# Optimization experiments

Hardware: AMD Instinct MI355X
Metric: run time of the kernel (lower is better)

The kernel has to match this reference:

```python
import jax, jax.numpy as jnp
import numpy as np

# LIF constants derived from init kwargs (delta_t=1e-3, tau_mem=20e-3, tau_syn=7.5e-3, tau_ref=2.86e-3)
THR = 1.0
ALPHA = float(np.exp(-1e-3 / 20e-3))   # membrane-trace decay for P
BETA = float(np.exp(-1e-3 / 7.5e-3))   # synaptic-trace decay for Q
GAMMA = float(np.exp(-1e-3 / 2.86e-3)) # refractory decay for R
POOL = 2
PAD = 2


def _conv2d(x, w, b):
    # x: [B,Cin,H,W], w: [Cout,Cin,k,k] -> [B,Cout,H,W] (same padding=2 for k=5)
    y = jax.lax.conv_general_dilated(
        x, w, window_strides=(1, 1), padding=[(PAD, PAD), (PAD, PAD)],
        dimension_numbers=('NCHW', 'OIHW', 'NCHW'))
    return y + b[None, :, None, None]


def _maxpool(x, k):
    return jax.lax.reduce_window(x, -jnp.inf, jax.lax.max,
                                 (1, 1, k, k), (1, 1, k, k), 'VALID')


def _spike(u):
    # hard threshold with SmoothStep (boxcar) straight-through surrogate gradient
    s_hard = (u > THR).astype(u.dtype)
    surr = jnp.clip(u - THR + 0.5, 0.0, 1.0)
    return jax.lax.stop_gradient(s_hard - surr) + surr


def setup_inputs() -> dict:
    key = jax.random.key(0)
    ks = jax.random.split(key, 7)
    B, Cin, H, W = 64, 64, 64, 64
    Cout, K = 128, 5
    fan_in = K * K * Cin
    flat = Cout * (H // POOL) * (W // POOL)  # 131072
    input_t = (jax.random.uniform(ks[0], (B, Cin, H, W)) < 0.1).astype(jnp.float32)
    P = jax.random.normal(ks[1], (B, Cin, H, W), jnp.float32)
    Q = jax.random.normal(ks[2], (B, Cin, H, W), jnp.float32)
    R = jax.random.normal(ks[3], (B, Cout, H, W), jnp.float32) * 0.1
    weights = jax.random.normal(ks[4], (Cout, Cin, K, K), jnp.float32) / np.sqrt(fan_in)
    bias = jax.random.normal(ks[5], (Cout,), jnp.float32) * 0.01
    L = 0.5 / np.sqrt(flat)  # lc_ampl / sqrt(input_features)
    w_sign = jax.random.uniform(ks[6], (10, flat), jnp.float32, -L, L)
    return {"input_t": input_t, "P": P, "Q": Q, "R": R,
            "weights": weights, "bias": bias, "w_sign": w_sign}


def reference(input_t, P, Q, R, weights, bias, w_sign):
    # one LIF timestep (quantization globals are None -> quant ops are identity, scale=1)
    P_new = ALPHA * P + (1.0 - ALPHA) * Q          # membrane trace
    Q_new = BETA * Q + (1.0 - BETA) * input_t      # synaptic trace
    R_new = GAMMA * R                              # refractory decay
    U = _conv2d(P_new, weights, bias) - R_new      # membrane potential
    S = _spike(U)                                  # spikes
    flat = _maxpool(S, POOL).reshape(S.shape[0], -1)
    # QLinearFunctional with sign random weights: (x @ W^T + 1)/2
    readout = (jnp.einsum('bf,of->bo', flat, w_sign) + 1.0) * 0.5
    return (S, U, readout)
```

## Files before the change

### kernel.cpp

```cpp
#include <hip/hip_runtime.h>
#include <math.h>

#define B_    64
#define CIN   64
#define COUT  128
#define HWHW  4096
#define NPIX  (B_ * COUT * HWHW)
#define TAU   2e-4f
#define NW3   204800
#define POOLED_FLOATS (B_ * COUT * 1024)
#define PART_FLOATS   (B_ * 10 * COUT)
#define PNS   66

typedef _Float16 half8  __attribute__((ext_vector_type(8)));
typedef _Float16 half2v __attribute__((ext_vector_type(2)));
typedef float    f32x4  __attribute__((ext_vector_type(4)));
typedef float    f32x16 __attribute__((ext_vector_type(16)));

__device__ __forceinline__ void gload_lds16(const void* g, void* l)
{
    __builtin_amdgcn_global_load_lds(
        (const __attribute__((address_space(1))) unsigned int*)g,
        (__attribute__((address_space(3))) unsigned int*)l, 16, 0, 0);
}

__global__ __launch_bounds__(256) void wprep_kernel(
    const float* __restrict__ W, _Float16* __restrict__ whi,
    _Float16* __restrict__ wlo)
{
    int e = blockIdx.x * 256 + threadIdx.x;
    if (e >= NW3) return;
    int k   = e & 15;
    int co  = (e >> 4) & 127;
    int r   = e >> 11;
    int tap = r % 25;
    int cc  = r / 25;
    float w = W[(size_t)((co << 6) + (cc << 4) + k) * 25 + tap];
    _Float16 h = (_Float16)w;
    whi[e] = h;
    wlo[e] = (_Float16)(w - (float)h);
}

__global__ __launch_bounds__(256) void pnprep_kernel(
    const float* __restrict__ P, const float* __restrict__ Q,
    _Float16* __restrict__ pnh, _Float16* __restrict__ pnl,
    float alpha, float oma)
{
    const int tid = threadIdx.x;
    const int y   = blockIdx.x;
    const int b   = blockIdx.y;
    __shared__ _Float16 th[64 * PNS];
    __shared__ _Float16 tl[64 * PNS];

    const size_t rb = (size_t)b * CIN * HWHW + ((size_t)y << 6);
#pragma unroll
    for (int k = 0; k < 4; ++k) {
        int idx = tid + (k << 8);
        int cin = idx >> 4;
        int x0  = (idx & 15) << 2;
        float4 p4 = *(const float4*)(P + rb + (size_t)cin * HWHW + x0);
        float4 q4 = *(const float4*)(Q + rb + (size_t)cin * HWHW + x0);
        float pn[4] = { alpha * p4.x + oma * q4.x, alpha * p4.y + oma * q4.y,
                        alpha * p4.z + oma * q4.z, alpha * p4.w + oma * q4.w };
        half2v h0, h1, l0, l1;
        {
            _Float16 a0 = (_Float16)pn[0], a1 = (_Float16)pn[1];
            _Float16 a2 = (_Float16)pn[2], a3 = (_Float16)pn[3];
            h0[0] = a0; h0[1] = a1; h1[0] = a2; h1[1] = a3;
            l0[0] = (_Float16)(pn[0] - (float)a0);
            l0[1] = (_Float16)(pn[1] - (float)a1);
            l1[0] = (_Float16)(pn[2] - (float)a2);
            l1[1] = (_Float16)(pn[3] - (float)a3);
        }
        int base = cin * PNS + x0;
        *(half2v*)&th[base]     = h0;
        *(half2v*)&th[base + 2] = h1;
        *(half2v*)&tl[base]     = l0;
        *(half2v*)&tl[base + 2] = l1;
    }
    __syncthreads();

    const size_t ob = ((((size_t)b << 12) + ((size_t)y << 6)) << 6);
#pragma unroll
    for (int k = 0; k < 2; ++k) {
        int gg  = tid + (k << 8);
        int x   = gg >> 3;
        int oct = gg & 7;
        half8 hv, lv;
#pragma unroll
        for (int j = 0; j < 8; ++j) {
            hv[j] = th[(oct * 8 + j) * PNS + x];
            lv[j] = tl[(oct * 8 + j) * PNS + x];
        }
        *(half8*)(pnh + ob + ((size_t)x << 6) + (oct << 3)) = hv;
        *(half8*)(pnl + ob + ((size_t)x << 6) + (oct << 3)) = lv;
    }
}

struct WFrag2 { half8 h[2]; half8 l[2]; };

__global__ __launch_bounds__(256) void lif_conv_mfma_pn_kernel(
    const _Float16* __restrict__ pnh, const _Float16* __restrict__ pnl,
    const float* __restrict__ R, const _Float16* __restrict__ whi,
    const _Float16* __restrict__ wlo, const float* __restrict__ bias,
    float* __restrict__ out, float* __restrict__ pooled,
    const void* __restrict__ zp,
    unsigned* __restrict__ cnt, int* __restrict__ list, int cap,
    float gamma)
{
    const int tid  = threadIdx.x;
    const int wave = tid >> 6;
    const int lane = tid & 63;
    const int b      = blockIdx.z;
    const int cobase = blockIdx.y << 6;
    const int ty0    = (blockIdx.x >> 2) << 4;
    const int tx0    = (blockIdx.x & 3) << 4;
    const int l31    = lane & 31;
    const int loct   = lane >> 5;

    __shared__ __align__(16) _Float16 sH[416 * 16];
    __shared__ __align__(16) _Float16 sL[416 * 16];

    f32x16 acc[2][2];
#pragma unroll
    for (int i = 0; i < 2; ++i)
#pragma unroll
        for (int j = 0; j < 2; ++j)
#pragma unroll
            for (int r = 0; r < 16; ++r) acc[i][j][r] = 0.f;

    const int wlb = ((cobase + l31) << 4) + (loct << 3);

    for (int cc = 0; cc < 4; ++cc) {
        __syncthreads();
        for (int i = wave; i < 26; i += 4) {
            const int ii = (i < 13) ? i : (i - 13);
            _Float16* sbuf = (i < 13) ? sH : sL;
            const _Float16* gb = (i < 13) ? pnh : pnl;
            const int g  = (ii << 6) + lane;
            const int px = g >> 1;
            const int c  = g & 1;
            const int r  = px / 20;
            const int col = px - 20 * r;
            const int gy = ty0 - 2 + r;
            const int gx = tx0 - 2 + col;
            const void* src = zp;
            if (px < 400 && (unsigned)gy < 64u && (unsigned)gx < 64u) {
                const int cs = c ^ ((px >> 2) & 1);
                src = gb + ((((size_t)b << 12) + (gy << 6) + gx) << 6)
                         + (cc << 4) + (cs << 3);
            }
            gload_lds16(src, (char*)sbuf + (ii << 10));
        }
        __syncthreads();

        const _Float16* wh  = whi + (size_t)cc * 25 * 2048 + wlb;
        const _Float16* wl_ = wlo + (size_t)cc * 25 * 2048 + wlb;
        WFrag2 wbuf[2];
#pragma unroll
        for (int nt = 0; nt < 2; ++nt) {
            wbuf[0].h[nt] = *(const half8*)(wh + (nt << 9));
            wbuf[0].l[nt] = *(const half8*)(wl_ + (nt << 9));
        }
#pragma unroll
        for (int t = 0; t < 25; ++t) {
            {
                const int tn = (t < 24) ? (t + 1) : 24;
                WFrag2& wn = wbuf[(t + 1) & 1];
#pragma unroll
                for (int nt = 0; nt < 2; ++nt) {
                    wn.h[nt] = *(const half8*)(wh + (size_t)tn * 2048 + (nt << 9));
                    wn.l[nt] = *(const half8*)(wl_ + (size_t)tn * 2048 + (nt << 9));
                }
            }
            __builtin_amdgcn_sched_barrier(0);

            const WFrag2& w = wbuf[t & 1];
            const int dy = t / 5;
            const int dx = t - 5 * dy;

            half8 aH[2], aL[2];
#pragma unroll
            for (int mt = 0; mt < 2; ++mt) {
                const int px = ((wave << 1) + mt) << 5 | l31;
                const int hp = ((px >> 4) + dy) * 20 + (px & 15) + dx;
                int a = (hp << 5) + (loct << 4);
                a ^= ((hp >> 2) & 1) << 4;
                aH[mt] = *(const half8*)((const char*)sH + a);
                aL[mt] = *(const half8*)((const char*)sL + a);
            }

            __builtin_amdgcn_s_setprio(1);
#pragma unroll
            for (int mt = 0; mt < 2; ++mt) {
#pragma unroll
                for (int nt = 0; nt < 2; ++nt) {
                    acc[mt][nt] = __builtin_amdgcn_mfma_f32_32x32x16_f16(
                        aH[mt], w.h[nt], acc[mt][nt], 0, 0, 0);
                    acc[mt][nt] = __builtin_amdgcn_mfma_f32_32x32x16_f16(
                        aH[mt], w.l[nt], acc[mt][nt], 0, 0, 0);
                    acc[mt][nt] = __builtin_amdgcn_mfma_f32_32x32x16_f16(
                        aL[mt], w.h[nt], acc[mt][nt], 0, 0, 0);
                }
            }
            __builtin_amdgcn_s_setprio(0);
        }
    }

#pragma unroll
    for (int nt = 0; nt < 2; ++nt) {
        const int co = cobase + (nt << 5) + l31;
        const float bv = bias[co];
        const int plane = b * COUT + co;
#pragma unroll
        for (int mt = 0; mt < 2; ++mt) {
            const int m = (wave << 1) + mt;
            float us[4][4];
#pragma unroll
            for (int rg = 0; rg < 4; ++rg) {
                const int y  = ty0 + (m << 1) + (rg >> 1);
                const int xb = ((rg & 1) << 3) + (loct << 2);
                const size_t ro = ((size_t)plane << 12) + (y << 6) + tx0 + xb;
                float4 r4 = *(const float4*)&R[ro];
                us[rg][0] = acc[mt][nt][(rg << 2) + 0] + bv - gamma * r4.x;
                us[rg][1] = acc[mt][nt][(rg << 2) + 1] + bv - gamma * r4.y;
                us[rg][2] = acc[mt][nt][(rg << 2) + 2] + bv - gamma * r4.z;
                us[rg][3] = acc[mt][nt][(rg << 2) + 3] + bv - gamma * r4.w;
                float4 uq = make_float4(us[rg][0], us[rg][1], us[rg][2], us[rg][3]);
                float4 sq = make_float4(us[rg][0] > 1.f ? 1.f : 0.f,
                                        us[rg][1] > 1.f ? 1.f : 0.f,
                                        us[rg][2] > 1.f ? 1.f : 0.f,
                                        us[rg][3] > 1.f ? 1.f : 0.f);
                *(float4*)&out[ro] = sq;
                *(float4*)&out[(size_t)NPIX + ro] = uq;
#pragma unroll
                for (int j = 0; j < 4; ++j) {
                    if (fabsf(us[rg][j] - 1.f) < TAU) {
                        unsigned pos = atomicAdd(cnt, 1u);
                        if (pos < (unsigned)cap)
                            list[pos] = (int)(ro + j);
                    }
                }
            }
            const int py  = (ty0 >> 1) + m;
            const int pxb = (tx0 >> 1) + (loct << 1);
            float* pp = pooled + ((size_t)plane << 10) + (py << 5);
            float2 pA, pB;
            pA.x = (fmaxf(fmaxf(us[0][0], us[0][1]), fmaxf(us[2][0], us[2][1])) > 1.f) ? 1.f : 0.f;
            pA.y = (fmaxf(fmaxf(us[0][2], us[0][3]), fmaxf(us[2][2], us[2][3])) > 1.f) ? 1.f : 0.f;
            pB.x = (fmaxf(fmaxf(us[1][0], us[1][1]), fmaxf(us[3][0], us[3][1])) > 1.f) ? 1.f : 0.f;
            pB.y = (fmaxf(fmaxf(us[1][2], us[1][3]), fmaxf(us[3][2], us[3][3])) > 1.f) ? 1.f : 0.f;
            *(float2*)(pp + pxb) = pA;
            *(float2*)(pp + pxb + 4) = pB;
        }
    }
}

__global__ __launch_bounds__(256) void lif_conv_mfma_reg_kernel(
    const float* __restrict__ P, const float* __restrict__ Q,
    const float* __restrict__ R, const _Float16* __restrict__ whi,
    const _Float16* __restrict__ wlo, const float* __restrict__ bias,
    float* __restrict__ out, float* __restrict__ pooled,
    unsigned* __restrict__ cnt, int* __restrict__ list, int cap, int do_pool,
    float alpha, float oma, float gamma)
{
    const int tid  = threadIdx.x;
    const int wave = tid >> 6;
    const int lane = tid & 63;
    const int b      = blockIdx.z;
    const int cobase = blockIdx.y << 6;
    const int ty0    = (blockIdx.x >> 2) << 4;
    const int tx0    = (blockIdx.x & 3) << 4;
    const int l31    = lane & 31;
    const int loct   = lane >> 5;

    __shared__ __align__(16) _Float16 sH[6400];
    __shared__ __align__(16) _Float16 sL[6400];

    f32x16 acc[2][2];
#pragma unroll
    for (int i = 0; i < 2; ++i)
#pragma unroll
        for (int j = 0; j < 2; ++j)
#pragma unroll
            for (int r = 0; r < 16; ++r) acc[i][j][r] = 0.f;

    const int wlb = ((cobase + l31) << 4) + (loct << 3);

    for (int cc = 0; cc < 4; ++cc) {
        __syncthreads();
        for (int e = tid; e < 1024; e += 256) {
            int px = e & 511;
            int hh = e >> 9;
            if (px >= 400) continue;
            int r  = px / 20;
            int c_ = px - 20 * r;
            int gy = ty0 - 2 + r;
            int gx = tx0 - 2 + c_;
            half8 hv, lv;
            if ((unsigned)gy < 64u && (unsigned)gx < 64u) {
                const size_t pb = ((size_t)(b * CIN + (cc << 4) + (hh << 3)) << 12)
                                + (gy << 6) + gx;
                const float* Pp = P + pb;
                const float* Qp = Q + pb;
#pragma unroll
                for (int j = 0; j < 8; ++j) {
                    float pn = alpha * Pp[j << 12] + oma * Qp[j << 12];
                    _Float16 h = (_Float16)pn;
                    hv[j] = h;
                    lv[j] = (_Float16)(pn - (float)h);
                }
            } else {
#pragma unroll
                for (int j = 0; j < 8; ++j) { hv[j] = (_Float16)0.f; lv[j] = (_Float16)0.f; }
            }
            int a = (px << 5) + (hh << 4);
            a ^= ((px >> 2) & 1) << 4;
            *(half8*)((char*)sH + a) = hv;
            *(half8*)((char*)sL + a) = lv;
        }
        __syncthreads();

        const _Float16* wh  = whi + (size_t)cc * 25 * 2048 + wlb;
        const _Float16* wl_ = wlo + (size_t)cc * 25 * 2048 + wlb;
        WFrag2 wbuf[2];
#pragma unroll
        for (int nt = 0; nt < 2; ++nt) {
            wbuf[0].h[nt] = *(const half8*)(wh + (nt << 9));
            wbuf[0].l[nt] = *(const half8*)(wl_ + (nt << 9));
        }
#pragma unroll
        for (int t = 0; t < 25; ++t) {
            {
                const int tn = (t < 24) ? (t + 1) : 24;
                WFrag2& wn = wbuf[(t + 1) & 1];
#pragma unroll
                for (int nt = 0; nt < 2; ++nt) {
                    wn.h[nt] = *(const half8*)(wh + (size_t)tn * 2048 + (nt << 9));
                    wn.l[nt] = *(const half8*)(wl_ + (size_t)tn * 2048 + (nt << 9));
                }
            }
            __builtin_amdgcn_sched_barrier(0);

            const WFrag2& w = wbuf[t & 1];
            const int dy = t / 5;
            const int dx = t - 5 * dy;
            half8 aH[2], aL[2];
#pragma unroll
            for (int mt = 0; mt < 2; ++mt) {
                const int px = ((wave << 1) + mt) << 5 | l31;
                const int hp = ((px >> 4) + dy) * 20 + (px & 15) + dx;
                int a = (hp << 5) + (loct << 4);
                a ^= ((hp >> 2) & 1) << 4;
                aH[mt] = *(const half8*)((const char*)sH + a);
                aL[mt] = *(const half8*)((const char*)sL + a);
            }
            __builtin_amdgcn_s_setprio(1);
#pragma unroll
            for (int mt = 0; mt < 2; ++mt) {
#pragma unroll
                for (int nt = 0; nt < 2; ++nt) {
                    acc[mt][nt] = __builtin_amdgcn_mfma_f32_32x32x16_f16(
                        aH[mt], w.h[nt], acc[mt][nt], 0, 0, 0);
                    acc[mt][nt] = __builtin_amdgcn_mfma_f32_32x32x16_f16(
                        aH[mt], w.l[nt], acc[mt][nt], 0, 0, 0);
                    acc[mt][nt] = __builtin_amdgcn_mfma_f32_32x32x16_f16(
                        aL[mt], w.h[nt], acc[mt][nt], 0, 0, 0);
                }
            }
            __builtin_amdgcn_s_setprio(0);
        }
    }

#pragma unroll
    for (int nt = 0; nt < 2; ++nt) {
        const int co = cobase + (nt << 5) + l31;
        const float bv = bias[co];
        const int plane = b * COUT + co;
#pragma unroll
        for (int mt = 0; mt < 2; ++mt) {
            const int m = (wave << 1) + mt;
            float us[4][4];
#pragma unroll
            for (int rg = 0; rg < 4; ++rg) {
                const int y  = ty0 + (m << 1) + (rg >> 1);
                const int xb = ((rg & 1) << 3) + (loct << 2);
                const size_t ro = ((size_t)plane << 12) + (y << 6) + tx0 + xb;
                float4 r4 = *(const float4*)&R[ro];
                us[rg][0] = acc[mt][nt][(rg << 2) + 0] + bv - gamma * r4.x;
                us[rg][1] = acc[mt][nt][(rg << 2) + 1] + bv - gamma * r4.y;
                us[rg][2] = acc[mt][nt][(rg << 2) + 2] + bv - gamma * r4.z;
                us[rg][3] = acc[mt][nt][(rg << 2) + 3] + bv - gamma * r4.w;
                float4 uq = make_float4(us[rg][0], us[rg][1], us[rg][2], us[rg][3]);
                float4 sq = make_float4(us[rg][0] > 1.f ? 1.f : 0.f,
                                        us[rg][1] > 1.f ? 1.f : 0.f,
                                        us[rg][2] > 1.f ? 1.f : 0.f,
                                        us[rg][3] > 1.f ? 1.f : 0.f);
                *(float4*)&out[ro] = sq;
                *(float4*)&out[(size_t)NPIX + ro] = uq;
#pragma unroll
                for (int j = 0; j < 4; ++j) {
                    if (fabsf(us[rg][j] - 1.f) < TAU) {
                        unsigned pos = atomicAdd(cnt, 1u);
                        if (pos < (unsigned)cap)
                            list[pos] = (int)(ro + j);
                    }
                }
            }
            if (do_pool) {
                const int py  = (ty0 >> 1) + m;
                const int pxb = (tx0 >> 1) + (loct << 1);
                float* pp = pooled + ((size_t)plane << 10) + (py << 5);
                float2 pA, pB;
                pA.x = (fmaxf(fmaxf(us[0][0], us[0][1]), fmaxf(us[2][0], us[2][1])) > 1.f) ? 1.f : 0.f;
                pA.y = (fmaxf(fmaxf(us[0][2], us[0][3]), fmaxf(us[2][2], us[2][3])) > 1.f) ? 1.f : 0.f;
                pB.x = (fmaxf(fmaxf(us[1][0], us[1][1]), fmaxf(us[3][0], us[3][1])) > 1.f) ? 1.f : 0.f;
                pB.y = (fmaxf(fmaxf(us[1][2], us[1][3]), fmaxf(us[3][2], us[3][3])) > 1.f) ? 1.f : 0.f;
                *(float2*)(pp + pxb) = pA;
                *(float2*)(pp + pxb + 4) = pB;
            }
        }
    }
}

__global__ __launch_bounds__(256) void repair_list_kernel(
    const float* __restrict__ P, const float* __restrict__ Q,
    const float* __restrict__ R, const float* __restrict__ W,
    const float* __restrict__ bias, float* __restrict__ out,
    const unsigned* __restrict__ cnt, const int* __restrict__ list, int cap,
    double alpha, double oma, double gamma)
{
    const int nrep = (int)min(*cnt, (unsigned)cap);
    const int wid  = (blockIdx.x * 256 + threadIdx.x) >> 6;
    const int lane = threadIdx.x & 63;
    const int nw   = (gridDim.x * 256) >> 6;

    for (int i = wid; i < nrep; i += nw) {
        const int idx   = list[i];
        const int plane = idx >> 12;
        const int pix   = idx & 4095;
        const int oy    = pix >> 6;
        const int ox    = pix & 63;
        const int b     = plane >> 7;
        const int co    = plane & 127;

        const float* Pp = P + ((size_t)b * CIN + lane) * HWHW;
        const float* Qp = Q + ((size_t)b * CIN + lane) * HWHW;
        const float* Wp = W + ((size_t)co * CIN + lane) * 25;

        double acc = 0.0;
#pragma unroll
        for (int dy = 0; dy < 5; ++dy) {
            int iy = oy + dy - 2;
            if ((unsigned)iy >= 64u) continue;
#pragma unroll
            for (int dx = 0; dx < 5; ++dx) {
                int ix = ox + dx - 2;
                if ((unsigned)ix >= 64u) continue;
                int off = (iy << 6) + ix;
                double pn = alpha * (double)Pp[off] + oma * (double)Qp[off];
                acc = fma((double)Wp[dy * 5 + dx], pn, acc);
            }
        }
#pragma unroll
        for (int s = 32; s; s >>= 1) acc += __shfl_down(acc, s, 64);

        if (lane == 0) {
            double u64 = acc + (double)bias[co]
                       - gamma * (double)R[(size_t)plane * HWHW + pix];
            out[idx]                = (u64 > 1.0) ? 1.f : 0.f;
            out[(size_t)NPIX + idx] = (float)u64;
        }
    }
}

__global__ __launch_bounds__(256) void pool_fix_kernel(
    const float* __restrict__ out, float* __restrict__ pooled,
    const unsigned* __restrict__ cnt, const int* __restrict__ list, int cap)
{
    const int nrep = (int)min(*cnt, (unsigned)cap);
    for (int i = blockIdx.x * 256 + threadIdx.x; i < nrep; i += gridDim.x * 256) {
        int idx   = list[i];
        int plane = idx >> 12;
        int pix   = idx & 4095;
        int oy    = pix >> 6;
        int ox    = pix & 63;
        size_t base = ((size_t)plane << 12) + ((oy & ~1) << 6) + (ox & ~1);
        float m = fmaxf(fmaxf(out[base], out[base + 1]),
                        fmaxf(out[base + 64], out[base + 65]));
        pooled[((size_t)plane << 10) + ((oy >> 1) << 5) + (ox >> 1)] = m;
    }
}

__global__ void ro_init(float* ro)
{
    int i = blockIdx.x * 256 + threadIdx.x;
    if (i < 640) ro[i] = 0.5f;
}

__global__ __launch_bounds__(256) void readout_pooled_kernel(
    const float* __restrict__ pooled, const float* __restrict__ wsig,
    float* __restrict__ part)
{
    const int tid = threadIdx.x;
    const int c   = blockIdx.x;
    const int bg  = blockIdx.y;

    __shared__ float wl[10 * 1024];
    for (int i = tid; i < 10240; i += 256)
        wl[i] = wsig[(size_t)(i >> 10) * 131072 + (c << 10) + (i & 1023)];
    __syncthreads();

    __shared__ float psum[4][10];
    const int wave = tid >> 6;
    const int lane = tid & 63;

    for (int bi = 0; bi < 8; ++bi) {
        const int b = (bg << 3) + bi;
        const float* pp = pooled + (((size_t)b * COUT + c) << 10);
        float acc[10];
#pragma unroll
        for (int o = 0; o < 10; ++o) acc[o] = 0.f;
#pragma unroll
        for (int it = 0; it < 4; ++it) {
            int f = tid + (it << 8);
            float m = pp[f];
#pragma unroll
            for (int o = 0; o < 10; ++o)
                acc[o] = fmaf(m, wl[(o << 10) + f], acc[o]);
        }
#pragma unroll
        for (int o = 0; o < 10; ++o) {
            float v = acc[o];
            v += __shfl_down(v, 32, 64);
            v += __shfl_down(v, 16, 64);
            v += __shfl_down(v, 8, 64);
            v += __shfl_down(v, 4, 64);
            v += __shfl_down(v, 2, 64);
            v += __shfl_down(v, 1, 64);
            if (lane == 0) psum[wave][o] = v;
        }
        __syncthreads();
        if (tid < 10) {
            float s = psum[0][tid] + psum[1][tid] + psum[2][tid] + psum[3][tid];
            part[((size_t)b * 10 + tid) * 128 + c] = s;
        }
        __syncthreads();
    }
}

__global__ __launch_bounds__(256) void readout_reduce_kernel(
    const float* __restrict__ part, float* __restrict__ ro)
{
    int i = blockIdx.x * 256 + threadIdx.x;
    if (i >= 640) return;
    const float* pp = part + (size_t)i * 128;
    float s = 0.f;
#pragma unroll
    for (int c = 0; c < 128; ++c) s += pp[c];
    ro[i] = 0.5f * s + 0.5f;
}

__global__ __launch_bounds__(256) void readout_kernel(
    const float* __restrict__ S, const float* __restrict__ wsig,
    float* __restrict__ ro)
{
    const int tid = threadIdx.x;
    const int b = blockIdx.x >> 7;
    const int c = blockIdx.x & 127;

    __shared__ float wl[10 * 1024];
    for (int idx = tid; idx < 10240; idx += 256) {
        int o = idx >> 10;
        int f = idx & 1023;
        wl[idx] = wsig[(size_t)o * 131072 + (c << 10) + f];
    }
    __syncthreads();

    float acc[10];
#pragma unroll
    for (int o = 0; o < 10; ++o) acc[o] = 0.f;

    const float* Sp = S + ((size_t)b * COUT + c) * HWHW;
#pragma unroll
    for (int i = 0; i < 4; ++i) {
        int fl = tid + (i << 8);
        int ph = fl >> 5, pw = fl & 31;
        const float2 t0 = *(const float2*)&Sp[(ph << 7) + (pw << 1)];
        const float2 t1 = *(const float2*)&Sp[(ph << 7) + 64 + (pw << 1)];
        float m = fmaxf(fmaxf(t0.x, t0.y), fmaxf(t1.x, t1.y));
#pragma unroll
        for (int o = 0; o < 10; ++o)
            acc[o] = fmaf(m, wl[(o << 10) + fl], acc[o]);
    }

    __shared__ float psum[4][10];
    const int wave = tid >> 6;
    const int lane = tid & 63;
#pragma unroll
    for (int o = 0; o < 10; ++o) {
        float v = acc[o];
        v += __shfl_down(v, 32, 64);
        v += __shfl_down(v, 16, 64);
        v += __shfl_down(v, 8, 64);
        v += __shfl_down(v, 4, 64);
        v += __shfl_down(v, 2, 64);
        v += __shfl_down(v, 1, 64);
        if (lane == 0) psum[wave][o] = v;
    }
    __syncthreads();
    if (tid < 10) {
        float s = psum[0][tid] + psum[1][tid] + psum[2][tid] + psum[3][tid];
        atomicAdd(&ro[b * 10 + tid], 0.5f * s);
    }
}

extern "C" void kernel_launch(void* const* d_in, const int* in_sizes, int n_in,
                              void* d_out, int out_size, void* d_ws, size_t ws_size,
                              hipStream_t stream)
{
    const float* P    = (const float*)d_in[1];
    const float* Q    = (const float*)d_in[2];
    const float* R    = (const float*)d_in[3];
    const float* W    = (const float*)d_in[4];
    const float* bias = (const float*)d_in[5];
    const float* wsig = (const float*)d_in[6];
    float* out = (float*)d_out;

    const size_t wbytes      = (size_t)NW3 * 2 * 2;
    const size_t pooled_bytes = (size_t)POOLED_FLOATS * 4;
    const size_t part_bytes   = (size_t)PART_FLOATS * 4;
    const size_t pn_bytes     = (size_t)B_ * CIN * HWHW * 2;

    const double alpha_d = exp(-1e-3 / 20e-3);
    const double oma_d   = 1.0 - alpha_d;
    const double gamma_d = exp(-1e-3 / 2.86e-3);

    size_t off = 4096;
    size_t pooled_off = off; off += pooled_bytes;
    size_t part_off   = off; off += part_bytes;
    size_t list_off   = off; off += ((size_t)4 << 20);
    size_t pnh_off    = off; off += pn_bytes;
    size_t pnl_off    = off; off += pn_bytes;
    size_t w_off      = off; off += wbytes + 256;
    const int use_pn = (ws_size >= off);

    if (use_pn) {
        unsigned* cnt = (unsigned*)d_ws;
        const void* zp = (const void*)((char*)d_ws + 256);
        float* pooled = (float*)((char*)d_ws + pooled_off);
        float* part   = (float*)((char*)d_ws + part_off);
        int*   list   = (int*)((char*)d_ws + list_off);
        int    cap    = (1 << 20);
        _Float16* pnh = (_Float16*)((char*)d_ws + pnh_off);
        _Float16* pnl = (_Float16*)((char*)d_ws + pnl_off);
        _Float16* whi = (_Float16*)((char*)d_ws + w_off);
        _Float16* wlo = whi + NW3;

        (void)hipMemsetAsync(d_ws, 0, 512, stream);

        wprep_kernel<<<(NW3 + 255) / 256, 256, 0, stream>>>(W, whi, wlo);
        pnprep_kernel<<<dim3(64, 64), 256, 0, stream>>>(P, Q, pnh, pnl,
                                                        (float)alpha_d, (float)oma_d);

        dim3 grid(16, 2, 64);
        lif_conv_mfma_pn_kernel<<<grid, 256, 0, stream>>>(pnh, pnl, R, whi, wlo,
                                                          bias, out, pooled, zp,
                                                          cnt, list, cap,
                                                          (float)gamma_d);

        repair_list_kernel<<<2048, 256, 0, stream>>>(P, Q, R, W, bias, out,
                                                     cnt, list, cap,
                                                     alpha_d, oma_d, gamma_d);
        pool_fix_kernel<<<64, 256, 0, stream>>>(out, pooled, cnt, list, cap);
        readout_pooled_kernel<<<dim3(128, 8), 256, 0, stream>>>(pooled, wsig, part);
        readout_reduce_kernel<<<3, 256, 0, stream>>>(part, out + (size_t)2 * NPIX);
        return;
    }

    size_t wsoff = (ws_size - wbytes) & ~(size_t)63;
    _Float16* whi = (_Float16*)((char*)d_ws + wsoff);
    _Float16* wlo = whi + NW3;
    unsigned* cnt = (unsigned*)d_ws;

    const int use_pooled = ws_size >= 64 + pooled_bytes + part_bytes
                                     + (1u << 22) + wbytes + 64;
    float* pooled = use_pooled ? (float*)((char*)d_ws + 64) : (float*)d_ws;
    float* part   = use_pooled ? (float*)((char*)d_ws + 64 + pooled_bytes)
                               : (float*)d_ws;
    size_t listoff = use_pooled ? (64 + pooled_bytes + part_bytes) : 16;
    int* list = (int*)((char*)d_ws + listoff);
    size_t cap_sz = (wsoff > listoff) ? (wsoff - listoff) / 4 : 0;
    int cap = (int)(cap_sz > (size_t)NPIX ? (size_t)NPIX : cap_sz);

    (void)hipMemsetAsync(d_ws, 0, 16, stream);

    wprep_kernel<<<(NW3 + 255) / 256, 256, 0, stream>>>(W, whi, wlo);

    dim3 grid(16, 2, 64);
    lif_conv_mfma_reg_kernel<<<grid, 256, 0, stream>>>(P, Q, R, whi, wlo, bias,
                                                       out, pooled, cnt, list, cap,
                                                       use_pooled,
                                                       (float)alpha_d, (float)oma_d,
                                                       (float)gamma_d);

    repair_list_kernel<<<2048, 256, 0, stream>>>(P, Q, R, W, bias, out,
                                                 cnt, list, cap,
                                                 alpha_d, oma_d, gamma_d);

    if (use_pooled) {
        pool_fix_kernel<<<64, 256, 0, stream>>>(out, pooled, cnt, list, cap);
        readout_pooled_kernel<<<dim3(128, 8), 256, 0, stream>>>(pooled, wsig, part);
        readout_reduce_kernel<<<3, 256, 0, stream>>>(part, out + (size_t)2 * NPIX);
    } else {
        float* ro = out + (size_t)2 * NPIX;
        ro_init<<<3, 256, 0, stream>>>(ro);
        readout_kernel<<<8192, 256, 0, stream>>>(out, wsig, ro);
    }
}
```

Before: 606.3 us.

## Double-buffer LDS activation fragments and switch to XOR-3bit LDS swizzle

Activation fragments for the conv MFMA loop are now loaded from LDS one tap ahead into a double buffer, so LDS reads overlap the current tap's MFMAs rather than sitting in front of them. The LDS swizzle changes from a 1-bit chunk swap folded into the global source address to a 3-bit XOR on the destination chunk index, which is meant to cut bank conflicts on the reads. The pixel base offsets are hoisted out of the loops. This costs extra VGPRs for the prefetched fragments, which may reduce occupancy.

After: 617.4 us. No clear change (+1.8%).

```diff
diff --git a/kernel.cpp b/kernel.cpp
--- a/kernel.cpp
+++ b/kernel.cpp
@@ -130,6 +130,12 @@
             for (int r = 0; r < 16; ++r) acc[i][j][r] = 0.f;
 
     const int wlb = ((cobase + l31) << 4) + (loct << 3);
+    int hp0[2];
+#pragma unroll
+    for (int mt = 0; mt < 2; ++mt) {
+        const int px = ((wave << 1) + mt) << 5 | l31;
+        hp0[mt] = (px >> 4) * 20 + (px & 15);
+    }
 
     for (int cc = 0; cc < 4; ++cc) {
         __syncthreads();
@@ -137,18 +143,18 @@
             const int ii = (i < 13) ? i : (i - 13);
             _Float16* sbuf = (i < 13) ? sH : sL;
             const _Float16* gb = (i < 13) ? pnh : pnl;
-            const int g  = (ii << 6) + lane;
-            const int px = g >> 1;
-            const int c  = g & 1;
+            const int d  = (ii << 6) + lane;
+            const int lg = d ^ ((d >> 3) & 7);
+            const int px = lg >> 1;
+            const int c  = lg & 1;
             const int r  = px / 20;
             const int col = px - 20 * r;
             const int gy = ty0 - 2 + r;
             const int gx = tx0 - 2 + col;
             const void* src = zp;
             if (px < 400 && (unsigned)gy < 64u && (unsigned)gx < 64u) {
-                const int cs = c ^ ((px >> 2) & 1);
                 src = gb + ((((size_t)b << 12) + (gy << 6) + gx) << 6)
-                         + (cc << 4) + (cs << 3);
+                         + (cc << 4) + (c << 3);
             }
             gload_lds16(src, (char*)sbuf + (ii << 10));
         }
@@ -157,15 +163,23 @@
         const _Float16* wh  = whi + (size_t)cc * 25 * 2048 + wlb;
         const _Float16* wl_ = wlo + (size_t)cc * 25 * 2048 + wlb;
         WFrag2 wbuf[2];
+        half8 aHb[2][2], aLb[2][2];
 #pragma unroll
         for (int nt = 0; nt < 2; ++nt) {
             wbuf[0].h[nt] = *(const half8*)(wh + (nt << 9));
             wbuf[0].l[nt] = *(const half8*)(wl_ + (nt << 9));
         }
 #pragma unroll
+        for (int mt = 0; mt < 2; ++mt) {
+            int g = (hp0[mt] << 1) + loct;
+            g ^= (g >> 3) & 7;
+            aHb[0][mt] = *(const half8*)((const char*)sH + (g << 4));
+            aLb[0][mt] = *(const half8*)((const char*)sL + (g << 4));
+        }
+#pragma unroll
         for (int t = 0; t < 25; ++t) {
+            const int tn = (t < 24) ? (t + 1) : 24;
             {
-                const int tn = (t < 24) ? (t + 1) : 24;
                 WFrag2& wn = wbuf[(t + 1) & 1];
 #pragma unroll
                 for (int nt = 0; nt < 2; ++nt) {
@@ -173,34 +187,31 @@
                     wn.l[nt] = *(const half8*)(wl_ + (size_t)tn * 2048 + (nt << 9));
                 }
             }
+            {
+                const int dyn = tn / 5;
+                const int dxn = tn - 5 * dyn;
+#pragma unroll
+                for (int mt = 0; mt < 2; ++mt) {
+                    int g = ((hp0[mt] + dyn * 20 + dxn) << 1) + loct;
+                    g ^= (g >> 3) & 7;
+                    aHb[(t + 1) & 1][mt] = *(const half8*)((const char*)sH + (g << 4));
+                    aLb[(t + 1) & 1][mt] = *(const half8*)((const char*)sL + (g << 4));
+                }
+            }
             __builtin_amdgcn_sched_barrier(0);
 
             const WFrag2& w = wbuf[t & 1];
-            const int dy = t / 5;
-            const int dx = t - 5 * dy;
-
-            half8 aH[2], aL[2];
-#pragma unroll
-            for (int mt = 0; mt < 2; ++mt) {
-                const int px = ((wave << 1) + mt) << 5 | l31;
-                const int hp = ((px >> 4) + dy) * 20 + (px & 15) + dx;
-                int a = (hp << 5) + (loct << 4);
-                a ^= ((hp >> 2) & 1) << 4;
-                aH[mt] = *(const half8*)((const char*)sH + a);
-                aL[mt] = *(const half8*)((const char*)sL + a);
-            }
-
             __builtin_amdgcn_s_setprio(1);
 #pragma unroll
             for (int mt = 0; mt < 2; ++mt) {
 #pragma unroll
                 for (int nt = 0; nt < 2; ++nt) {
                     acc[mt][nt] = __builtin_amdgcn_mfma_f32_32x32x16_f16(
-                        aH[mt], w.h[nt], acc[mt][nt], 0, 0, 0);
+                        aHb[t & 1][mt], w.h[nt], acc[mt][nt], 0, 0, 0);
                     acc[mt][nt] = __builtin_amdgcn_mfma_f32_32x32x16_f16(
-                        aH[mt], w.l[nt], acc[mt][nt], 0, 0, 0);
+                        aHb[t & 1][mt], w.l[nt], acc[mt][nt], 0, 0, 0);
                     acc[mt][nt] = __builtin_amdgcn_mfma_f32_32x32x16_f16(
-                        aL[mt], w.h[nt], acc[mt][nt], 0, 0, 0);
+                        aLb[t & 1][mt], w.h[nt], acc[mt][nt], 0, 0, 0);
                 }
             }
             __builtin_amdgcn_s_setprio(0);
```
